# Kernel tuning notes

Measured on AMD Instinct MI355X. Metric: run time of the kernel, lower is better.

The kernel has to match this reference:

```python
import jax, jax.numpy as jnp
import numpy as np

DIM = 768
EPS = 1e-06


def _layernorm(x, gamma, beta):
    # LayerNorm over last axis (channels), eps=EPS, elementwise affine
    mu = jnp.mean(x, axis=-1, keepdims=True)
    var = jnp.mean(jnp.square(x - mu), axis=-1, keepdims=True)
    return (x - mu) * jax.lax.rsqrt(var + EPS) * gamma + beta


def setup_inputs() -> dict:
    key = jax.random.key(0)
    ks = jax.random.split(key, 10)
    B, C, H, W = 16, DIM, 32, 32
    s = 1.0 / np.sqrt(C)  # mimic Conv2d default init scale
    return {
        "x": jax.random.normal(ks[0], (B, C, H, W), dtype=jnp.float32),
        "W1": jax.random.uniform(ks[1], (C, C), jnp.float32, -s, s),
        "b1": jax.random.uniform(ks[2], (C,), jnp.float32, -s, s),
        "g1": jnp.ones((C,), jnp.float32),
        "beta1": jnp.zeros((C,), jnp.float32),
        "W2": jax.random.uniform(ks[3], (C, C), jnp.float32, -s, s),
        "b2": jax.random.uniform(ks[4], (C,), jnp.float32, -s, s),
        "g2": jnp.ones((C,), jnp.float32),
        "beta2": jnp.zeros((C,), jnp.float32),
        "W3": jax.random.uniform(ks[5], (C, C), jnp.float32, -s, s),
        "b3": jax.random.uniform(ks[6], (C,), jnp.float32, -s, s),
    }


def reference(x, W1, b1, g1, beta1, W2, b2, g2, beta2, W3, b3):
    # x: [B, C, H, W] (NCHW). Work in NHWC; 1x1 conv == channel matmul.
    h = jnp.transpose(x, (0, 2, 3, 1))  # [B, H, W, C]
    h = jnp.einsum("bhwc,oc->bhwo", h, W1) + b1
    h = jax.nn.gelu(_layernorm(h, g1, beta1), approximate=False)
    h = jnp.einsum("bhwc,oc->bhwo", h, W2) + b2
    h = jax.nn.gelu(_layernorm(h, g2, beta2), approximate=False)
    h = jnp.einsum("bhwc,oc->bhwo", h, W3) + b3
    return jnp.transpose(h, (0, 3, 1, 2))  # back to NCHW
```

## Files before the change

### kernel.cpp

```cpp
#include <hip/hip_runtime.h>
#include <hip/hip_bf16.h>

typedef __bf16 bf16;
typedef __bf16 bf16x4 __attribute__((ext_vector_type(4)));
typedef __bf16 bf16x8 __attribute__((ext_vector_type(8)));
typedef float f32x4 __attribute__((ext_vector_type(4)));

#define DIM 768
#define HW 1024
#define BATCH 16
#define M_TOTAL (BATCH * HW)
#define NKT 12

#define AS1 __attribute__((address_space(1)))
#define AS3 __attribute__((address_space(3)))


__global__ void wcvt3_kernel(const float4* __restrict__ w1, const float4* __restrict__ w2,
                             const float4* __restrict__ w3,
                             bf16x8* __restrict__ o1, bf16x8* __restrict__ o2,
                             bf16x8* __restrict__ o3) {
    const int b = blockIdx.x;
    const int which = b / 288;
    const int i = (b % 288) * 256 + threadIdx.x;
    const float4* w = which == 0 ? w1 : which == 1 ? w2 : w3;
    bf16x8* o = which == 0 ? o1 : which == 1 ? o2 : o3;
    const int row = i / 96, br = i % 96;
    const int q = br >> 2, g = br & 3;
    float4 lo = w[row * 192 + q * 8 + g];
    float4 hi = w[row * 192 + q * 8 + g + 4];
    bf16x8 r = { (bf16)lo.x, (bf16)lo.y, (bf16)lo.z, (bf16)lo.w,
                 (bf16)hi.x, (bf16)hi.y, (bf16)hi.z, (bf16)hi.w };
    o[row * 96 + br] = r;
}

__global__ void transpose_cvt_kernel(const float* __restrict__ x, bf16* __restrict__ xb) {
    __shared__ float tile[32][33];
    const int b = blockIdx.z;
    const int hw0 = blockIdx.x * 32;
    const int c0 = blockIdx.y * 32;
    const int tx = threadIdx.x, ty = threadIdx.y;

    const float* src = x + ((size_t)b * DIM + c0) * HW + hw0;
#pragma unroll
    for (int j = 0; j < 4; j++)
        tile[ty + 8 * j][tx] = src[(size_t)(ty + 8 * j) * HW + tx];
    __syncthreads();
    const int ptx = (((tx & 15) >> 2) << 3) + (tx & 3) + ((tx >> 4) << 2);
    bf16* dst = xb + ((size_t)b * HW + hw0) * DIM + c0;
#pragma unroll
    for (int j = 0; j < 4; j++)
        dst[(size_t)(ty + 8 * j) * DIM + ptx] = (bf16)tile[tx][ty + 8 * j];
}

template <int MODE>
__global__ __launch_bounds__(512, 2) void gemm_kernel(
    const bf16* __restrict__ A,
    const bf16* __restrict__ Bw,
    const float* __restrict__ bias,
    void* __restrict__ out)
{
    constexpr int K = DIM;
    __shared__ bf16 lds[2][2][256][64];

    const int t = threadIdx.x;
    const int lane = t & 63;
    const int wave = t >> 6;
    const int wm = wave >> 2, wn = wave & 3;

    const int bid = blockIdx.x;
    const int swz = (bid & 7) * 24 + (bid >> 3);
    const int m0 = (swz % 64) * 256;
    const int n0 = (swz / 64) * 256;

    const int fr = lane & 15;
    const int fq = lane >> 4;

    f32x4 acc[8][4] = {};

    const int s_r = t >> 3;
    const int s_blk = t & 7;

    auto stage_half = [&](int kt, int which, int half) {
        const int d = kt & 1;
        const bf16* src = which == 0 ? A : Bw;
        const int row0 = which == 0 ? m0 : n0;
#pragma unroll
        for (int j = 0; j < 2; j++) {
            const int r = s_r + j * 64;
            const int R = half * 128 + r;
            __builtin_amdgcn_global_load_lds(
                (const AS1 void*)(src + (size_t)(row0 + R) * K + kt * 64 + ((s_blk ^ (r & 7)) << 3)),
                (AS3 void*)&lds[d][which][R][s_blk * 8], 16, 0, 0);
        }
    };

    bf16x8 a[8], b0[4], b1[4];

    auto ldA = [&](int kt, int mh) {
        const int d = kt & 1;
#pragma unroll
        for (int mi = 0; mi < 4; mi++) {
            const int R = wm * 128 + (mh * 4 + mi) * 16 + fr;
            const bf16* rp = &lds[d][0][R][0];
            const int s = R & 7;
#pragma unroll
            for (int ks = 0; ks < 2; ks++)
                a[mi * 2 + ks] = *(const bf16x8*)(rp + (((ks * 4 + fq) ^ s) << 3));
        }
    };
    auto ldB = [&](bf16x8* bb, int kt, int nh) {
        const int d = kt & 1;
#pragma unroll
        for (int ni = 0; ni < 2; ni++) {
            const int R = wn * 64 + (nh * 2 + ni) * 16 + fr;
            const bf16* rp = &lds[d][1][R][0];
            const int s = R & 7;
#pragma unroll
            for (int ks = 0; ks < 2; ks++)
                bb[ni * 2 + ks] = *(const bf16x8*)(rp + (((ks * 4 + fq) ^ s) << 3));
        }
    };
    auto MM = [&](bf16x8* bb, int mh, int nh) {
        __builtin_amdgcn_s_setprio(1);
#pragma unroll
        for (int mi = 0; mi < 4; mi++)
#pragma unroll
            for (int ni = 0; ni < 2; ni++)
#pragma unroll
                for (int ks = 0; ks < 2; ks++)
                    acc[mh * 4 + mi][nh * 2 + ni] = __builtin_amdgcn_mfma_f32_16x16x32_bf16(
                        a[mi * 2 + ks], bb[ni * 2 + ks], acc[mh * 4 + mi][nh * 2 + ni], 0, 0, 0);
        __builtin_amdgcn_s_setprio(0);
    };

    stage_half(0, 0, 0); stage_half(0, 0, 1); stage_half(0, 1, 0); stage_half(0, 1, 1);
    stage_half(1, 0, 0);
    asm volatile("s_waitcnt vmcnt(2)" ::: "memory");
    __builtin_amdgcn_s_barrier();

    for (int kt = 0; kt < NKT; ++kt) {
        ldA(kt, 0);
        ldB(b0, kt, 0);
        if (kt + 1 < NKT) stage_half(kt + 1, 0, 1);
        __builtin_amdgcn_s_barrier();
        asm volatile("s_waitcnt lgkmcnt(0)" ::: "memory");
        MM(b0, 0, 0);
        __builtin_amdgcn_s_barrier();
        ldB(b1, kt, 1);
        if (kt + 1 < NKT) stage_half(kt + 1, 1, 0);
        __builtin_amdgcn_s_barrier();
        asm volatile("s_waitcnt lgkmcnt(0)" ::: "memory");
        MM(b1, 0, 1);
        __builtin_amdgcn_s_barrier();
        ldA(kt, 1);
        if (kt + 1 < NKT) stage_half(kt + 1, 1, 1);
        __builtin_amdgcn_s_barrier();
        asm volatile("s_waitcnt lgkmcnt(0)" ::: "memory");
        MM(b1, 1, 1);
        __builtin_amdgcn_s_barrier();
        if (kt + 2 < NKT) stage_half(kt + 2, 0, 0);
        MM(b0, 1, 0);
        if (kt < NKT - 2) { asm volatile("s_waitcnt vmcnt(2)" ::: "memory"); }
        else if (kt == NKT - 2) { asm volatile("s_waitcnt vmcnt(0)" ::: "memory"); }
        __builtin_amdgcn_s_barrier();
    }

    const int fq4 = fq * 4;
    if (MODE == 0) {
        bf16* o = (bf16*)out;
#pragma unroll
        for (int mi = 0; mi < 8; mi++) {
            const int row = m0 + wm * 128 + mi * 16 + fq4;
#pragma unroll
            for (int ni = 0; ni < 4; ni++) {
                const int col = n0 + wn * 64 + ni * 16 + fr;
                const int pcol = n0 + wn * 64 + ((ni >> 1) << 5)
                               + ((fr >> 2) << 3) + (fr & 3) + ((ni & 1) << 2);
                const float bv = bias[col];
#pragma unroll
                for (int r = 0; r < 4; r++)
                    o[(size_t)(row + r) * DIM + pcol] = (bf16)(acc[mi][ni][r] + bv);
            }
        }
    } else {
        float* o = (float*)out;
#pragma unroll
        for (int mi = 0; mi < 8; mi++) {
            const int nb = m0 + wm * 128 + mi * 16 + fq4;
            const int bI = nb >> 10, hw = nb & 1023;
#pragma unroll
            for (int ni = 0; ni < 4; ni++) {
                const int col = n0 + wn * 64 + ni * 16 + fr;
                f32x4 v = acc[mi][ni] + bias[col];
                *(f32x4*)(o + ((size_t)bI * DIM + col) * HW + hw) = v;
            }
        }
    }
}

__global__ __launch_bounds__(256) void ln_gelu_kernel(
    bf16* __restrict__ h, const float* __restrict__ g, const float* __restrict__ beta)
{
    const int wave = threadIdx.x >> 6;
    const int lane = threadIdx.x & 63;
    const int n = blockIdx.x * 4 + wave;
    bf16* row = h + (size_t)n * DIM;

    float v[12];
    float s = 0.f, ss = 0.f;
#pragma unroll
    for (int j = 0; j < 3; j++) {
        bf16x4 x = *(const bf16x4*)(row + j * 256 + lane * 4);
#pragma unroll
        for (int i = 0; i < 4; i++) {
            float f = (float)x[i];
            v[j * 4 + i] = f;
            s += f;
            ss += f * f;
        }
    }
#pragma unroll
    for (int off = 32; off > 0; off >>= 1) {
        s += __shfl_xor(s, off);
        ss += __shfl_xor(ss, off);
    }
    const float mu = s * (1.f / DIM);
    const float var = ss * (1.f / DIM) - mu * mu;
    const float rstd = rsqrtf(var + 1e-6f);

#pragma unroll
    for (int j = 0; j < 3; j++) {
        bf16x4 r;
#pragma unroll
        for (int i = 0; i < 4; i++) {
            const int c = j * 256 + lane * 4 + i;
            const int p = (lane * 4 + i) & 31;
            const int kk = ((p >> 3) << 2) + (p & 7) + ((p & 4) ? 12 : 0);
            const int gi = (c & ~31) + kk;
            float y = (v[j * 4 + i] - mu) * rstd * g[gi] + beta[gi];
            y = 0.5f * y * (1.f + erff(y * 0.70710678118f));
            r[i] = (bf16)y;
        }
        *(bf16x4*)(row + j * 256 + lane * 4) = r;
    }
}

extern "C" void kernel_launch(void* const* d_in, const int* in_sizes, int n_in,
                              void* d_out, int out_size, void* d_ws, size_t ws_size,
                              hipStream_t stream) {
    const float* x   = (const float*)d_in[0];
    const float* W1  = (const float*)d_in[1];
    const float* b1  = (const float*)d_in[2];
    const float* g1  = (const float*)d_in[3];
    const float* be1 = (const float*)d_in[4];
    const float* W2  = (const float*)d_in[5];
    const float* b2  = (const float*)d_in[6];
    const float* g2  = (const float*)d_in[7];
    const float* be2 = (const float*)d_in[8];
    const float* W3  = (const float*)d_in[9];
    const float* b3  = (const float*)d_in[10];
    float* out = (float*)d_out;

    bf16* Wb1  = (bf16*)d_ws;
    bf16* Wb2  = Wb1 + (size_t)DIM * DIM;
    bf16* Wb3  = Wb2 + (size_t)DIM * DIM;
    bf16* buf0 = Wb3 + (size_t)DIM * DIM;
    bf16* buf1 = buf0 + (size_t)M_TOTAL * DIM;

    wcvt3_kernel<<<864, 256, 0, stream>>>((const float4*)W1, (const float4*)W2, (const float4*)W3,
                                          (bf16x8*)Wb1, (bf16x8*)Wb2, (bf16x8*)Wb3);

    transpose_cvt_kernel<<<dim3(32, 24, 16), dim3(32, 8), 0, stream>>>(x, buf0);

    const int ggrid = (M_TOTAL / 256) * (DIM / 256);
    gemm_kernel<0><<<ggrid, 512, 0, stream>>>(buf0, Wb1, b1, buf1);
    ln_gelu_kernel<<<M_TOTAL / 4, 256, 0, stream>>>(buf1, g1, be1);
    gemm_kernel<0><<<ggrid, 512, 0, stream>>>(buf1, Wb2, b2, buf0);
    ln_gelu_kernel<<<M_TOTAL / 4, 256, 0, stream>>>(buf0, g2, be2);
    gemm_kernel<1><<<ggrid, 512, 0, stream>>>(buf0, Wb3, b3, out);
}
```

Measured before the change: 158.6 us.

## Merge prep kernels and drop redundant barriers in GEMM main loop

Combines the weight-conversion and input transpose/convert kernels into one launch, saving a kernel launch and tail. In the GEMM K-loop, most workgroup barriers between LDS reads and MFMA phases are removed, leaving one barrier before the next-stage write plus a conditional barrier at the end of each iteration. A sched_barrier is added to keep the compiler from reordering across iterations. This cuts synchronisation stalls but risks LDS read/write races if the remaining barriers do not cover every buffer-reuse hazard.

```diff
diff --git a/kernel.cpp b/kernel.cpp
--- a/kernel.cpp
+++ b/kernel.cpp
@@ -16,41 +16,44 @@
 #define AS3 __attribute__((address_space(3)))
 
 
-__global__ void wcvt3_kernel(const float4* __restrict__ w1, const float4* __restrict__ w2,
-                             const float4* __restrict__ w3,
-                             bf16x8* __restrict__ o1, bf16x8* __restrict__ o2,
-                             bf16x8* __restrict__ o3) {
-    const int b = blockIdx.x;
-    const int which = b / 288;
-    const int i = (b % 288) * 256 + threadIdx.x;
-    const float4* w = which == 0 ? w1 : which == 1 ? w2 : w3;
-    bf16x8* o = which == 0 ? o1 : which == 1 ? o2 : o3;
-    const int row = i / 96, br = i % 96;
-    const int q = br >> 2, g = br & 3;
-    float4 lo = w[row * 192 + q * 8 + g];
-    float4 hi = w[row * 192 + q * 8 + g + 4];
-    bf16x8 r = { (bf16)lo.x, (bf16)lo.y, (bf16)lo.z, (bf16)lo.w,
-                 (bf16)hi.x, (bf16)hi.y, (bf16)hi.z, (bf16)hi.w };
-    o[row * 96 + br] = r;
-}
-
-__global__ void transpose_cvt_kernel(const float* __restrict__ x, bf16* __restrict__ xb) {
+__global__ void prep_kernel(const float* __restrict__ x, bf16* __restrict__ xb,
+                            const float4* __restrict__ w1, const float4* __restrict__ w2,
+                            const float4* __restrict__ w3,
+                            bf16x8* __restrict__ o1, bf16x8* __restrict__ o2,
+                            bf16x8* __restrict__ o3) {
     __shared__ float tile[32][33];
-    const int b = blockIdx.z;
-    const int hw0 = blockIdx.x * 32;
-    const int c0 = blockIdx.y * 32;
-    const int tx = threadIdx.x, ty = threadIdx.y;
-
-    const float* src = x + ((size_t)b * DIM + c0) * HW + hw0;
-#pragma unroll
-    for (int j = 0; j < 4; j++)
-        tile[ty + 8 * j][tx] = src[(size_t)(ty + 8 * j) * HW + tx];
-    __syncthreads();
-    const int ptx = (((tx & 15) >> 2) << 3) + (tx & 3) + ((tx >> 4) << 2);
-    bf16* dst = xb + ((size_t)b * HW + hw0) * DIM + c0;
-#pragma unroll
-    for (int j = 0; j < 4; j++)
-        dst[(size_t)(ty + 8 * j) * DIM + ptx] = (bf16)tile[tx][ty + 8 * j];
+    if (blockIdx.x < 864) {
+        const int b = blockIdx.x;
+        const int which = b / 288;
+        const int i = (b % 288) * 256 + threadIdx.x;
+        const float4* w = which == 0 ? w1 : which == 1 ? w2 : w3;
+        bf16x8* o = which == 0 ? o1 : which == 1 ? o2 : o3;
+        const int row = i / 96, br = i % 96;
+        const int q = br >> 2, g = br & 3;
+        float4 lo = w[row * 192 + q * 8 + g];
+        float4 hi = w[row * 192 + q * 8 + g + 4];
+        bf16x8 r = { (bf16)lo.x, (bf16)lo.y, (bf16)lo.z, (bf16)lo.w,
+                     (bf16)hi.x, (bf16)hi.y, (bf16)hi.z, (bf16)hi.w };
+        o[row * 96 + br] = r;
+    } else {
+        const int e = blockIdx.x - 864;
+        const int b = e / 768;
+        const int rem = e % 768;
+        const int c0 = (rem / 32) * 32;
+        const int hw0 = (rem % 32) * 32;
+        const int tx = threadIdx.x & 31, ty = threadIdx.x >> 5;
+
+        const float* src = x + ((size_t)b * DIM + c0) * HW + hw0;
+#pragma unroll
+        for (int j = 0; j < 4; j++)
+            tile[ty + 8 * j][tx] = src[(size_t)(ty + 8 * j) * HW + tx];
+        __syncthreads();
+        const int ptx = (((tx & 15) >> 2) << 3) + (tx & 3) + ((tx >> 4) << 2);
+        bf16* dst = xb + ((size_t)b * HW + hw0) * DIM + c0;
+#pragma unroll
+        for (int j = 0; j < 4; j++)
+            dst[(size_t)(ty + 8 * j) * DIM + ptx] = (bf16)tile[tx][ty + 8 * j];
+    }
 }
 
 template <int MODE>
@@ -143,27 +146,31 @@
         ldA(kt, 0);
         ldB(b0, kt, 0);
         if (kt + 1 < NKT) stage_half(kt + 1, 0, 1);
-        __builtin_amdgcn_s_barrier();
         asm volatile("s_waitcnt lgkmcnt(0)" ::: "memory");
         MM(b0, 0, 0);
-        __builtin_amdgcn_s_barrier();
+
         ldB(b1, kt, 1);
         if (kt + 1 < NKT) stage_half(kt + 1, 1, 0);
-        __builtin_amdgcn_s_barrier();
         asm volatile("s_waitcnt lgkmcnt(0)" ::: "memory");
         MM(b1, 0, 1);
-        __builtin_amdgcn_s_barrier();
+
         ldA(kt, 1);
         if (kt + 1 < NKT) stage_half(kt + 1, 1, 1);
-        __builtin_amdgcn_s_barrier();
         asm volatile("s_waitcnt lgkmcnt(0)" ::: "memory");
         MM(b1, 1, 1);
+
         __builtin_amdgcn_s_barrier();
         if (kt + 2 < NKT) stage_half(kt + 2, 0, 0);
         MM(b0, 1, 0);
-        if (kt < NKT - 2) { asm volatile("s_waitcnt vmcnt(2)" ::: "memory"); }
-        else if (kt == NKT - 2) { asm volatile("s_waitcnt vmcnt(0)" ::: "memory"); }
-        __builtin_amdgcn_s_barrier();
+
+        if (kt < NKT - 2) {
+            asm volatile("s_waitcnt vmcnt(2)" ::: "memory");
+            __builtin_amdgcn_s_barrier();
+        } else if (kt == NKT - 2) {
+            asm volatile("s_waitcnt vmcnt(0)" ::: "memory");
+            __builtin_amdgcn_s_barrier();
+        }
+        __builtin_amdgcn_sched_barrier(0);
     }
 
     const int fq4 = fq * 4;
@@ -268,10 +275,9 @@
     bf16* buf0 = Wb3 + (size_t)DIM * DIM;
     bf16* buf1 = buf0 + (size_t)M_TOTAL * DIM;
 
-    wcvt3_kernel<<<864, 256, 0, stream>>>((const float4*)W1, (const float4*)W2, (const float4*)W3,
-                                          (bf16x8*)Wb1, (bf16x8*)Wb2, (bf16x8*)Wb3);
-
-    transpose_cvt_kernel<<<dim3(32, 24, 16), dim3(32, 8), 0, stream>>>(x, buf0);
+    prep_kernel<<<864 + 12288, 256, 0, stream>>>(
+        x, buf0, (const float4*)W1, (const float4*)W2, (const float4*)W3,
+        (bf16x8*)Wb1, (bf16x8*)Wb2, (bf16x8*)Wb3);
 
     const int ggrid = (M_TOTAL / 256) * (DIM / 256);
     gemm_kernel<0><<<ggrid, 512, 0, stream>>>(buf0, Wb1, b1, buf1);
```

Result: faster. 150.7 us (-5.0%).
